# Kernel tuning notes

Hardware: AMD Instinct MI355X
Metric: run time of the kernel (lower is better)

## Reference

```python
import jax, jax.numpy as jnp
import numpy as np

VOCAB = 1024
PRED_H = 320
ENC_H = 1024
JOINT_H = 640


def setup_inputs() -> dict:
    key = jax.random.key(0)
    k_f, k_g, k_w1, k_b1, k_w2, k_b2 = jax.random.split(key, 6)
    B, T, U = 8, 256, 65
    f = jax.random.normal(k_f, (B, T, ENC_H), dtype=jnp.float32)
    g = jax.random.normal(k_g, (B, U, PRED_H), dtype=jnp.float32)
    in_dim = PRED_H + ENC_H
    s1 = 1.0 / np.sqrt(in_dim)
    s2 = 1.0 / np.sqrt(JOINT_H)
    # W1 acts on cat([f, g], axis=-1): rows [0:ENC_H] hit f, rows [ENC_H:] hit g
    W1 = jax.random.uniform(k_w1, (in_dim, JOINT_H), minval=-s1, maxval=s1, dtype=jnp.float32)
    b1 = jax.random.uniform(k_b1, (JOINT_H,), minval=-s1, maxval=s1, dtype=jnp.float32)
    W2 = jax.random.uniform(k_w2, (JOINT_H, VOCAB), minval=-s2, maxval=s2, dtype=jnp.float32)
    b2 = jax.random.uniform(k_b2, (VOCAB,), minval=-s2, maxval=s2, dtype=jnp.float32)
    return {"f": f, "g": g, "W1": W1, "b1": b1, "W2": W2, "b2": b2}


def reference(f, g, W1, b1, W2, b2):
    # Linear(cat(f_expand, g_expand)) == f @ W1[:ENC_H] + g @ W1[ENC_H:] + b1,
    # broadcast-added over (T, U). Same math as the torch module (dropout p=0 / eval).
    W1f = W1[:ENC_H]          # (ENC_H, JOINT_H)
    W1g = W1[ENC_H:]          # (PRED_H, JOINT_H)
    hf = jnp.einsum("bth,hj->btj", f, W1f)            # (B, T, J)
    hg = jnp.einsum("buh,hj->buj", g, W1g)            # (B, U, J)
    h = jax.nn.relu(hf[:, :, None, :] + hg[:, None, :, :] + b1)  # (B, T, U, J)
    logits = jnp.einsum("btuj,jk->btuk", h, W2) + b2  # (B, T, U, VOCAB)
    return logits
```

## Files before the change

kernel.cpp:

```cpp
#include <hip/hip_runtime.h>
#include <cstdint>

typedef __bf16 bf16;
typedef __bf16 bf16x8 __attribute__((ext_vector_type(8)));
typedef float  f32x4  __attribute__((ext_vector_type(4)));

#define BARRIER()    asm volatile("s_barrier" ::: "memory")
#define WAIT_LGKM0() asm volatile("s_waitcnt lgkmcnt(0)" ::: "memory")
#define WAIT_VM(n)   asm volatile("s_waitcnt vmcnt(" #n ")" ::: "memory")

__device__ void gemm_small_body(
    const float* __restrict__ A, const float* __restrict__ Bm,
    const float* __restrict__ bias, bf16* __restrict__ Cout,
    int M, int N, int K, int bx, int by)
{
    __shared__ float As[64][20];
    __shared__ float Bs[16][68];
    const int tid = threadIdx.x;
    const int m0 = bx * 64, n0 = by * 64;
    const int tx = tid & 15, ty = tid >> 4;
    const int arow = tid >> 2, ak = (tid & 3) << 2;
    const int bk = tid >> 4, bc = (tid & 15) << 2;
    const bool avalid = (m0 + arow) < M;
    float acc[4][4] = {};

    for (int k0 = 0; k0 < K; k0 += 16) {
        float4 av = make_float4(0.f, 0.f, 0.f, 0.f);
        if (avalid) av = *(const float4*)&A[(size_t)(m0 + arow) * K + k0 + ak];
        float4 bv = *(const float4*)&Bm[(size_t)(k0 + bk) * N + n0 + bc];
        __syncthreads();
        *(float4*)&As[arow][ak] = av;
        *(float4*)&Bs[bk][bc] = bv;
        __syncthreads();
#pragma unroll
        for (int k = 0; k < 16; ++k) {
            float a[4], b[4];
#pragma unroll
            for (int i = 0; i < 4; ++i) a[i] = As[ty * 4 + i][k];
#pragma unroll
            for (int j = 0; j < 4; ++j) b[j] = Bs[k][tx * 4 + j];
#pragma unroll
            for (int i = 0; i < 4; ++i)
#pragma unroll
                for (int j = 0; j < 4; ++j) acc[i][j] += a[i] * b[j];
        }
    }
#pragma unroll
    for (int i = 0; i < 4; ++i) {
        int row = m0 + ty * 4 + i;
        if (row >= M) continue;
#pragma unroll
        for (int j = 0; j < 4; ++j) {
            int col = n0 + tx * 4 + j;
            float v = acc[i][j] + (bias ? bias[col] : 0.f);
            Cout[(size_t)row * N + col] = (bf16)v;
        }
    }
}

__device__ void w2t_body(const float* __restrict__ W2, bf16* __restrict__ W2T,
                         int bx, int by)
{
    __shared__ float t[32][33];
    const int tx = threadIdx.x & 31, ty = threadIdx.x >> 5;
    const int n0 = bx * 32, k0 = by * 32;
#pragma unroll
    for (int i = 0; i < 4; ++i)
        t[ty + i * 8][tx] = W2[(size_t)(k0 + ty + i * 8) * 1024 + n0 + tx];
    __syncthreads();
#pragma unroll
    for (int i = 0; i < 4; ++i)
        W2T[(size_t)(n0 + ty + i * 8) * 640 + k0 + tx] = (bf16)t[tx][ty + i * 8];
}

__global__ __launch_bounds__(256) void prep(
    const float* __restrict__ f, const float* __restrict__ g,
    const float* __restrict__ W1, const float* __restrict__ b1,
    const float* __restrict__ W2,
    bf16* __restrict__ hf, bf16* __restrict__ hgb, bf16* __restrict__ W2T)
{
    const int bid = blockIdx.x;
    if (bid < 320) {
        gemm_small_body(f, W1, nullptr, hf, 2048, 640, 1024, bid % 32, bid / 32);
    } else if (bid < 410) {
        int b = bid - 320;
        gemm_small_body(g, W1 + 1024 * 640, b1, hgb, 520, 640, 320, b % 9, b / 9);
    } else {
        int b = bid - 410;
        w2t_body(W2, W2T, b % 32, b / 32);
    }
}

__global__ __launch_bounds__(256, 3) void joint_main(
    const bf16* __restrict__ hf, const bf16* __restrict__ hgb,
    const bf16* __restrict__ W2T, const float* __restrict__ b2,
    float* __restrict__ out)
{
    __shared__ bf16 As[128 * 64];
    __shared__ bf16 Bs[128 * 64];
    const int tid = threadIdx.x;
    const int n0 = blockIdx.x * 128;
    const int m0 = blockIdx.y * 128;

    const int r  = tid >> 1;
    const int kh = (tid & 1) << 5;
    const int c0 = (tid & 1) << 2;
    int aoff[4];
#pragma unroll
    for (int c = 0; c < 4; ++c)
        aoff[c] = r * 64 + (((c0 + c) ^ (r & 7)) << 3);

    const int m  = m0 + r;
    const int bt = m / 65;
    const int uu = m - bt * 65;
    const int bb = bt >> 8;
    const bf16* hfp = hf  + (size_t)bt * 640 + kh;
    const bf16* hgp = hgb + (size_t)(bb * 65 + uu) * 640 + kh;

    const int wid = tid >> 6, lane = tid & 63;
    const int wr = wid >> 1, wc = wid & 1;
    const int lg = lane >> 4, l15 = lane & 15;

    f32x4 acc[4][4] = {};
    bf16x8 F[4], G[4];

    auto loadA = [&](int k0) {
#pragma unroll
        for (int i = 0; i < 2; ++i) {
            F[i] = *(const bf16x8*)(hfp + k0 + i * 8);
            G[i] = *(const bf16x8*)(hgp + k0 + i * 8);
        }
#pragma unroll
        for (int i = 2; i < 4; ++i) {
            F[i] = *(const bf16x8*)(hfp + k0 + i * 8);
            G[i] = *(const bf16x8*)(hgp + k0 + i * 8);
        }
    };
    auto stageB = [&](int k0) {
        const char* w2b = (const char*)W2T + (size_t)k0 * 2;
#pragma unroll
        for (int call = 0; call < 4; ++call) {
            int chunk = call * 256 + tid;
            int brow = chunk >> 3, c = chunk & 7;
            const char* src = w2b + (size_t)(n0 + brow) * 1280
                                  + ((c ^ (brow & 7)) << 4);
            __builtin_amdgcn_global_load_lds(
                (const __attribute__((address_space(1))) uint32_t*)src,
                (__attribute__((address_space(3))) uint32_t*)&Bs[chunk << 3],
                16, 0, 0);
        }
    };
    auto genA = [&]() {
#pragma unroll
        for (int c = 0; c < 4; ++c) {
            bf16x8 O;
#pragma unroll
            for (int i = 0; i < 8; ++i) {
                float s = (float)F[c][i] + (float)G[c][i];
                O[i] = (bf16)fmaxf(s, 0.f);
            }
            *(bf16x8*)&As[aoff[c]] = O;
        }
    };
    auto mfmaPhase = [&]() {
#pragma unroll
        for (int kk = 0; kk < 2; ++kk) {
            const int clog = (kk << 2) + lg;
            bf16x8 bfr[4], afr[4];
#pragma unroll
            for (int ni = 0; ni < 4; ++ni) {
                int row = wc * 64 + ni * 16 + l15;
                bfr[ni] = *(const bf16x8*)&Bs[row * 64 + ((clog ^ (row & 7)) << 3)];
            }
#pragma unroll
            for (int mi = 0; mi < 4; ++mi) {
                int row = wr * 64 + mi * 16 + l15;
                afr[mi] = *(const bf16x8*)&As[row * 64 + ((clog ^ (row & 7)) << 3)];
            }
#pragma unroll
            for (int mi = 0; mi < 4; ++mi)
#pragma unroll
                for (int ni = 0; ni < 4; ++ni)
                    acc[mi][ni] = __builtin_amdgcn_mfma_f32_16x16x32_bf16(
                        afr[mi], bfr[ni], acc[mi][ni], 0, 0, 0);
        }
    };

    loadA(0);
    stageB(0);

#pragma unroll 1
    for (int t = 0; t < 10; ++t) {
        genA();
        if (t < 9) loadA((t + 1) * 64);
        if (t < 9) { WAIT_VM(8); } else { WAIT_VM(0); }
        WAIT_LGKM0();
        BARRIER();
        mfmaPhase();
        BARRIER();
        if (t < 9) stageB((t + 1) * 64);
    }

    float bv[4];
#pragma unroll
    for (int ni = 0; ni < 4; ++ni) bv[ni] = b2[n0 + wc * 64 + ni * 16 + l15];
#pragma unroll
    for (int mi = 0; mi < 4; ++mi) {
#pragma unroll
        for (int ni = 0; ni < 4; ++ni) {
            int col = n0 + wc * 64 + ni * 16 + l15;
#pragma unroll
            for (int j = 0; j < 4; ++j) {
                int row = m0 + wr * 64 + mi * 16 + lg * 4 + j;
                out[(size_t)row * 1024 + col] = acc[mi][ni][j] + bv[ni];
            }
        }
    }
}

extern "C" void kernel_launch(void* const* d_in, const int* in_sizes, int n_in,
                              void* d_out, int out_size, void* d_ws, size_t ws_size,
                              hipStream_t stream)
{
    const float* f  = (const float*)d_in[0];
    const float* g  = (const float*)d_in[1];
    const float* W1 = (const float*)d_in[2];
    const float* b1 = (const float*)d_in[3];
    const float* W2 = (const float*)d_in[4];
    const float* b2 = (const float*)d_in[5];
    float* out = (float*)d_out;

    bf16* hf  = (bf16*)d_ws;
    bf16* hgb = hf + 2048 * 640;
    bf16* W2T = hgb + 520 * 640;

    prep<<<1050, 256, 0, stream>>>(f, g, W1, b1, W2, hf, hgb, W2T);
    joint_main<<<dim3(8, 1040), 256, 0, stream>>>(hf, hgb, W2T, b2, out);
}
```

Baseline: 325.6 us.

## Double-buffer W2T LDS tiles and raise wave priority during MFMA

The W2T tile moves to two LDS buffers, so the next K-slice is staged with global_load_lds before the current MFMA phase instead of after the second barrier. This lets the B-tile loads overlap the matrix multiply, and the vmcnt wait is adjusted to leave the prefetch in flight. s_setprio is raised around the MFMA phase so waves doing math are favoured by the scheduler. The extra 16KB of LDS per block may cut occupancy below the three blocks per CU that the launch bounds request.

```diff
diff --git a/kernel.cpp b/kernel.cpp
--- a/kernel.cpp
+++ b/kernel.cpp
@@ -97,7 +97,7 @@
     float* __restrict__ out)
 {
     __shared__ bf16 As[128 * 64];
-    __shared__ bf16 Bs[128 * 64];
+    __shared__ bf16 Bs[2][128 * 64];
     const int tid = threadIdx.x;
     const int n0 = blockIdx.x * 128;
     const int m0 = blockIdx.y * 128;
@@ -126,17 +126,12 @@
 
     auto loadA = [&](int k0) {
 #pragma unroll
-        for (int i = 0; i < 2; ++i) {
+        for (int i = 0; i < 4; ++i) {
             F[i] = *(const bf16x8*)(hfp + k0 + i * 8);
             G[i] = *(const bf16x8*)(hgp + k0 + i * 8);
         }
-#pragma unroll
-        for (int i = 2; i < 4; ++i) {
-            F[i] = *(const bf16x8*)(hfp + k0 + i * 8);
-            G[i] = *(const bf16x8*)(hgp + k0 + i * 8);
-        }
-    };
-    auto stageB = [&](int k0) {
+    };
+    auto stageB = [&](int buf, int k0) {
         const char* w2b = (const char*)W2T + (size_t)k0 * 2;
 #pragma unroll
         for (int call = 0; call < 4; ++call) {
@@ -146,7 +141,7 @@
                                   + ((c ^ (brow & 7)) << 4);
             __builtin_amdgcn_global_load_lds(
                 (const __attribute__((address_space(1))) uint32_t*)src,
-                (__attribute__((address_space(3))) uint32_t*)&Bs[chunk << 3],
+                (__attribute__((address_space(3))) uint32_t*)&Bs[buf][chunk << 3],
                 16, 0, 0);
         }
     };
@@ -162,7 +157,8 @@
             *(bf16x8*)&As[aoff[c]] = O;
         }
     };
-    auto mfmaPhase = [&]() {
+    auto mfmaPhase = [&](int buf) {
+        __builtin_amdgcn_s_setprio(1);
 #pragma unroll
         for (int kk = 0; kk < 2; ++kk) {
             const int clog = (kk << 2) + lg;
@@ -170,7 +166,7 @@
 #pragma unroll
             for (int ni = 0; ni < 4; ++ni) {
                 int row = wc * 64 + ni * 16 + l15;
-                bfr[ni] = *(const bf16x8*)&Bs[row * 64 + ((clog ^ (row & 7)) << 3)];
+                bfr[ni] = *(const bf16x8*)&Bs[buf][row * 64 + ((clog ^ (row & 7)) << 3)];
             }
 #pragma unroll
             for (int mi = 0; mi < 4; ++mi) {
@@ -184,21 +180,27 @@
                     acc[mi][ni] = __builtin_amdgcn_mfma_f32_16x16x32_bf16(
                         afr[mi], bfr[ni], acc[mi][ni], 0, 0, 0);
         }
+        __builtin_amdgcn_s_setprio(0);
     };
 
     loadA(0);
-    stageB(0);
+    stageB(0, 0);
 
 #pragma unroll 1
     for (int t = 0; t < 10; ++t) {
+        const int bufB = t & 1;
         genA();
-        if (t < 9) loadA((t + 1) * 64);
-        if (t < 9) { WAIT_VM(8); } else { WAIT_VM(0); }
+        if (t < 9) {
+            loadA((t + 1) * 64);
+            stageB(bufB ^ 1, (t + 1) * 64);
+            WAIT_VM(12);
+        } else {
+            WAIT_VM(0);
+        }
         WAIT_LGKM0();
         BARRIER();
-        mfmaPhase();
+        mfmaPhase(bufB);
         BARRIER();
-        if (t < 9) stageB((t + 1) * 64);
     }
 
     float bv[4];
```

New measurement: 331.9 us. About the same (+1.9%).

## Materialize relu(hf+hg) in workspace and stream both GEMM operands via DMA to LDS

Applied to the files above, without the earlier changes.

A new kernel writes the full (B*T*U, 640) bf16 relu(hf+hg) activation to workspace. The joint GEMM then loads both A and B tiles with global_load_lds into double-buffered LDS, replacing the register-based A generation and single-buffered pipeline. It also remaps blocks across XCDs and raises MFMA priority. The cost is about 170MB of extra HBM write plus read for the intermediate, in exchange for simpler, better-overlapped loads. The old path is kept as a fallback when the workspace is too small.

```diff
diff --git a/kernel.cpp b/kernel.cpp
--- a/kernel.cpp
+++ b/kernel.cpp
@@ -91,6 +91,137 @@
     }
 }
 
+__global__ __launch_bounds__(256) void hgen(
+    const bf16* __restrict__ hf, const bf16* __restrict__ hgb,
+    bf16* __restrict__ h)
+{
+    const uint32_t base = blockIdx.x * 5120u;
+#pragma unroll 4
+    for (int i = 0; i < 20; ++i) {
+        uint32_t chunk = base + i * 256u + threadIdx.x;
+        uint32_t r = chunk / 80u;
+        uint32_t c = chunk - r * 80u;
+        uint32_t bt = r / 65u;
+        uint32_t uu = r - bt * 65u;
+        uint32_t bb = bt >> 8;
+        bf16x8 F = *(const bf16x8*)(hf  + (size_t)bt * 640 + c * 8);
+        bf16x8 G = *(const bf16x8*)(hgb + (size_t)(bb * 65 + uu) * 640 + c * 8);
+        bf16x8 O;
+#pragma unroll
+        for (int j = 0; j < 8; ++j) {
+            float s = (float)F[j] + (float)G[j];
+            O[j] = (bf16)fmaxf(s, 0.f);
+        }
+        *(bf16x8*)(h + (size_t)r * 640 + c * 8) = O;
+    }
+}
+
+__global__ __launch_bounds__(256, 2) void joint_dma(
+    const bf16* __restrict__ h, const bf16* __restrict__ W2T,
+    const float* __restrict__ b2, float* __restrict__ out)
+{
+    __shared__ bf16 As[2][128 * 64];
+    __shared__ bf16 Bs[2][128 * 64];
+    const int tid = threadIdx.x;
+
+    const int d   = blockIdx.x;
+    const int xcd = d & 7;
+    const int s   = d >> 3;
+    const int n0  = (s & 7) * 128;
+    const int m0  = (((s >> 3) << 3) + xcd) * 128;
+
+    const int r0 = tid >> 3;
+    const int c  = tid & 7;
+    const int csw = (c ^ (r0 & 7)) << 4;
+    const char* asrc[4];
+    const char* bsrc[4];
+#pragma unroll
+    for (int call = 0; call < 4; ++call) {
+        asrc[call] = (const char*)h   + (size_t)(m0 + r0 + call * 32) * 1280 + csw;
+        bsrc[call] = (const char*)W2T + (size_t)(n0 + r0 + call * 32) * 1280 + csw;
+    }
+
+    const int wid = tid >> 6, lane = tid & 63;
+    const int wr = wid >> 1, wc = wid & 1;
+    const int lg = lane >> 4, l15 = lane & 15;
+
+    f32x4 acc[4][4] = {};
+
+    auto stage = [&](int buf, int k0) {
+        const size_t kb = (size_t)k0 * 2;
+#pragma unroll
+        for (int call = 0; call < 4; ++call) {
+            int chunk = call * 256 + tid;
+            __builtin_amdgcn_global_load_lds(
+                (const __attribute__((address_space(1))) uint32_t*)(asrc[call] + kb),
+                (__attribute__((address_space(3))) uint32_t*)&As[buf][chunk << 3],
+                16, 0, 0);
+        }
+#pragma unroll
+        for (int call = 0; call < 4; ++call) {
+            int chunk = call * 256 + tid;
+            __builtin_amdgcn_global_load_lds(
+                (const __attribute__((address_space(1))) uint32_t*)(bsrc[call] + kb),
+                (__attribute__((address_space(3))) uint32_t*)&Bs[buf][chunk << 3],
+                16, 0, 0);
+        }
+    };
+    auto mfmaPhase = [&](int buf) {
+#pragma unroll
+        for (int kk = 0; kk < 2; ++kk) {
+            const int clog = (kk << 2) + lg;
+            bf16x8 bfr[4], afr[4];
+#pragma unroll
+            for (int ni = 0; ni < 4; ++ni) {
+                int row = wc * 64 + ni * 16 + l15;
+                bfr[ni] = *(const bf16x8*)&Bs[buf][row * 64 + ((clog ^ (row & 7)) << 3)];
+            }
+#pragma unroll
+            for (int mi = 0; mi < 4; ++mi) {
+                int row = wr * 64 + mi * 16 + l15;
+                afr[mi] = *(const bf16x8*)&As[buf][row * 64 + ((clog ^ (row & 7)) << 3)];
+            }
+            __builtin_amdgcn_s_setprio(1);
+#pragma unroll
+            for (int mi = 0; mi < 4; ++mi)
+#pragma unroll
+                for (int ni = 0; ni < 4; ++ni)
+                    acc[mi][ni] = __builtin_amdgcn_mfma_f32_16x16x32_bf16(
+                        afr[mi], bfr[ni], acc[mi][ni], 0, 0, 0);
+            __builtin_amdgcn_s_setprio(0);
+        }
+    };
+
+    stage(0, 0);
+    WAIT_VM(0);
+    BARRIER();
+
+#pragma unroll 1
+    for (int t = 0; t < 10; ++t) {
+        const int cur = t & 1;
+        if (t < 9) stage(cur ^ 1, (t + 1) * 64);
+        mfmaPhase(cur);
+        WAIT_VM(0);
+        BARRIER();
+    }
+
+    float bv[4];
+#pragma unroll
+    for (int ni = 0; ni < 4; ++ni) bv[ni] = b2[n0 + wc * 64 + ni * 16 + l15];
+#pragma unroll
+    for (int mi = 0; mi < 4; ++mi) {
+#pragma unroll
+        for (int ni = 0; ni < 4; ++ni) {
+            int col = n0 + wc * 64 + ni * 16 + l15;
+#pragma unroll
+            for (int j = 0; j < 4; ++j) {
+                int row = m0 + wr * 64 + mi * 16 + lg * 4 + j;
+                out[(size_t)row * 1024 + col] = acc[mi][ni][j] + bv[ni];
+            }
+        }
+    }
+}
+
 __global__ __launch_bounds__(256, 3) void joint_main(
     const bf16* __restrict__ hf, const bf16* __restrict__ hgb,
     const bf16* __restrict__ W2T, const float* __restrict__ b2,
@@ -126,12 +257,7 @@
 
     auto loadA = [&](int k0) {
 #pragma unroll
-        for (int i = 0; i < 2; ++i) {
-            F[i] = *(const bf16x8*)(hfp + k0 + i * 8);
-            G[i] = *(const bf16x8*)(hgp + k0 + i * 8);
-        }
-#pragma unroll
-        for (int i = 2; i < 4; ++i) {
+        for (int i = 0; i < 4; ++i) {
             F[i] = *(const bf16x8*)(hfp + k0 + i * 8);
             G[i] = *(const bf16x8*)(hgp + k0 + i * 8);
         }
@@ -233,7 +359,16 @@
     bf16* hf  = (bf16*)d_ws;
     bf16* hgb = hf + 2048 * 640;
     bf16* W2T = hgb + 520 * 640;
+    bf16* h   = W2T + 1024 * 640;
+
+    const size_t need = ((size_t)(2048 + 520 + 1024) + 133120) * 640 * 2;
 
     prep<<<1050, 256, 0, stream>>>(f, g, W1, b1, W2, hf, hgb, W2T);
-    joint_main<<<dim3(8, 1040), 256, 0, stream>>>(hf, hgb, W2T, b2, out);
-}
+
+    if (ws_size >= need) {
+        hgen<<<2080, 256, 0, stream>>>(hf, hgb, h);
+        joint_dma<<<8320, 256, 0, stream>>>(h, W2T, b2, out);
+    } else {
+        joint_main<<<dim3(8, 1040), 256, 0, stream>>>(hf, hgb, W2T, b2, out);
+    }
+}
```

Measured after the change: 452.6 us. 1.39x slower.
